# Optimization experiments

Measured on AMD Instinct MI355X. Metric: run time of the kernel, lower is better.

Reference implementation:

```python
import jax, jax.numpy as jnp
import numpy as np
from jax import lax

DIM = 192
NUM_HEADS = 4
HEAD_DIM = DIM // NUM_HEADS
EPS_NORM = 1e-12  # F.normalize default eps
EPS_TEMP = 1e-06


def setup_inputs() -> dict:
    key = jax.random.key(0)
    k1, k2, k3, k4 = jax.random.split(key, 4)
    b, c, h, w = 2, DIM, 192, 192
    x = jax.random.normal(k1, (b, c, h, w), dtype=jnp.float32)
    # conv weights, fan-in scaled for sane magnitudes
    w_qkv = jax.random.normal(k2, (3 * DIM, DIM), dtype=jnp.float32) / np.sqrt(DIM)
    w_dw = jax.random.normal(k3, (3 * DIM, 1, 3, 3), dtype=jnp.float32) / 3.0
    w_proj = jax.random.normal(k4, (DIM, DIM), dtype=jnp.float32) / np.sqrt(DIM)
    log_temperature = jnp.zeros((NUM_HEADS, 1, 1), dtype=jnp.float32)
    return {"x": x, "w_qkv": w_qkv, "w_dw": w_dw, "w_proj": w_proj,
            "log_temperature": log_temperature}


def _l2norm_lastdim(t):
    n = jnp.sqrt(jnp.sum(t * t, axis=-1, keepdims=True))
    return t / jnp.maximum(n, EPS_NORM)


def reference(x, w_qkv, w_dw, w_proj, log_temperature):
    b, c, h, w = x.shape
    hw = h * w
    # 1x1 conv (pointwise GEMM over channels)
    qkv = jnp.einsum('oc,bchw->bohw', w_qkv, x)
    # depthwise 3x3 conv, padding=1
    qkv = lax.conv_general_dilated(
        qkv, w_dw, window_strides=(1, 1), padding='SAME',
        feature_group_count=3 * c,
        dimension_numbers=('NCHW', 'OIHW', 'NCHW'))
    q, k, v = jnp.split(qkv, 3, axis=1)
    # [b, heads, head_dim, hw]
    q = q.reshape(b, NUM_HEADS, HEAD_DIM, hw)
    k = k.reshape(b, NUM_HEADS, HEAD_DIM, hw)
    v = v.reshape(b, NUM_HEADS, HEAD_DIM, hw)
    q = _l2norm_lastdim(q)
    k = _l2norm_lastdim(k)
    # channel-wise attention: [b, heads, head_dim, head_dim]
    attn = jnp.einsum('bhdn,bhen->bhde', q, k)
    temperature = jax.nn.softplus(log_temperature) + EPS_TEMP  # [heads,1,1]
    attn = attn * temperature[None]
    attn = jax.nn.softmax(attn, axis=-1)
    out = jnp.einsum('bhde,bhen->bhdn', attn, v)
    out = out.reshape(b, c, h, w)
    return jnp.einsum('oc,bchw->bohw', w_proj, out)
```

## Files before the change

### kernel.cpp

```cpp
#include <hip/hip_runtime.h>
#include <math.h>

#define HW 36864
#define CC 192

typedef __attribute__((ext_vector_type(4))) float f32x4;
typedef __attribute__((ext_vector_type(8))) short bf16x8;

__device__ __forceinline__ float bf2f(unsigned short u) {
    return __uint_as_float(((unsigned int)u) << 16);
}
__device__ __forceinline__ unsigned short f2bf(float f) {
    unsigned int u = __float_as_uint(f);
    unsigned int r = (u + 0x7fffu + ((u >> 16) & 1u)) >> 16;
    return (unsigned short)r;
}

template<bool OUTBF, int NT, int NZ>
__global__ __launch_bounds__(256, 3) void gemm_rpa(
    const unsigned short* __restrict__ A,
    const unsigned short* __restrict__ X,
    void* __restrict__ Outv,
    long aBatchStride, long xBatchStride, long oBatchStride)
{
    const int nx = gridDim.x;
    int bx = blockIdx.x;
    if ((nx & 7) == 0) {
        const int cpx = nx >> 3;
        bx = (bx & 7) * cpx + (bx >> 3);
    }
    const int z  = (NZ > 1) ? (bx % NZ) : 0;
    const int ng = (NZ > 1) ? (bx / NZ) : bx;
    const int b  = blockIdx.y;
    const int mbase = z * 192;
    const int n00 = ng * (NT * 64);

    const int tid = threadIdx.x;
    const int lane = tid & 63;
    const int wave = tid >> 6;
    const int ml = lane & 15, qk = lane >> 4;
    const int kp = tid & 31;
    const int nc = tid >> 5;

    __shared__ __attribute__((aligned(16))) unsigned short Xs[64 * 202];

    const unsigned short* Ab = A + (long)b * aBatchStride;
    bf16x8 afr[3][6];
#pragma unroll
    for (int f = 0; f < 3; ++f) {
        const unsigned short* row = Ab + (long)(mbase + wave * 48 + f * 16 + ml) * 192 + qk * 8;
#pragma unroll
        for (int kk = 0; kk < 6; ++kk)
            afr[f][kk] = *(const bf16x8*)(row + kk * 32);
    }

    const unsigned short* Xg = X + (long)b * xBatchStride + n00 + nc * 8;

    f32x4 acc[3][4];
#pragma unroll
    for (int f = 0; f < 3; ++f)
#pragma unroll
        for (int s = 0; s < 4; ++s)
            acc[f][s] = (f32x4){0.f, 0.f, 0.f, 0.f};

    auto LOAD = [&](int g, int4* r) {
        const int t = g / 3, sec = g - 3 * t;
        const unsigned short* p = Xg + (long)(sec * 64 + 2 * kp) * HW + t * 64;
        r[0] = *(const int4*)(p);
        r[1] = *(const int4*)(p + HW);
    };
    auto WRITE = [&](int g, const int4* r) {
        const int t = g / 3, sec = g - 3 * t;
        const int k = sec * 64 + 2 * kp;
        const unsigned short* u0 = (const unsigned short*)&r[0];
        const unsigned short* u1 = (const unsigned short*)&r[1];
#pragma unroll
        for (int j = 0; j < 8; ++j)
            *(unsigned int*)&Xs[(nc * 8 + j) * 202 + k] =
                (unsigned int)u0[j] | ((unsigned int)u1[j] << 16);
    };
    auto COMPUTE = [&](int g) {
        const int sec = g % 3;
#pragma unroll
        for (int s = 0; s < 4; ++s) {
#pragma unroll
            for (int kl = 0; kl < 2; ++kl) {
                bf16x8 bfr;
                {
                    const unsigned short* p = &Xs[(s * 16 + ml) * 202 + sec * 64 + kl * 32 + qk * 8];
                    union { bf16x8 v; unsigned int u[4]; } tmp;
                    tmp.u[0] = *(const unsigned int*)(p + 0);
                    tmp.u[1] = *(const unsigned int*)(p + 2);
                    tmp.u[2] = *(const unsigned int*)(p + 4);
                    tmp.u[3] = *(const unsigned int*)(p + 6);
                    bfr = tmp.v;
                }
#pragma unroll
                for (int f = 0; f < 3; ++f)
                    acc[f][s] = __builtin_amdgcn_mfma_f32_16x16x32_bf16(afr[f][sec * 2 + kl], bfr, acc[f][s], 0, 0, 0);
            }
        }
    };
    auto STORE = [&](int t) {
        const int n0 = n00 + t * 64;
#pragma unroll
        for (int f = 0; f < 3; ++f) {
#pragma unroll
            for (int s = 0; s < 4; ++s) {
                const int gm = mbase + wave * 48 + f * 16 + qk * 4;
                const int gn = n0 + s * 16 + ml;
#pragma unroll
                for (int i = 0; i < 4; ++i) {
                    if (OUTBF)
                        ((unsigned short*)Outv)[(long)b * oBatchStride + (long)(gm + i) * HW + gn] = f2bf(acc[f][s][i]);
                    else
                        ((float*)Outv)[(long)b * oBatchStride + (long)(gm + i) * HW + gn] = acc[f][s][i];
                }
                acc[f][s] = (f32x4){0.f, 0.f, 0.f, 0.f};
            }
        }
    };

    constexpr int NS = NT * 3;
    int4 sA[2], sB[2];

    LOAD(0, sA);
    WRITE(0, sA);
    LOAD(1, sB);
    __syncthreads();

#pragma unroll
    for (int g = 0; g < NS; ++g) {
        if ((g & 1) == 0) {
            if (g + 2 < NS) LOAD(g + 2, sA);
            COMPUTE(g);
            if (g + 1 < NS) WRITE(g + 1, sB);
        } else {
            if (g + 2 < NS) LOAD(g + 2, sB);
            COMPUTE(g);
            if (g + 1 < NS) WRITE(g + 1, sA);
        }
        if (g % 3 == 2) STORE(g / 3);
        if (g + 1 < NS) __syncthreads();
    }
}

__global__ __launch_bounds__(256) void dwconv_kernel(
    const unsigned short* __restrict__ qkv,
    const float* __restrict__ wdw,
    unsigned short* __restrict__ dwout,
    float* __restrict__ ssq)
{
    const int ht = blockIdx.x;
    const int ch = blockIdx.y;
    const int b  = blockIdx.z;
    const int tid = threadIdx.x;
    const int lane = tid & 63;
    const int h0 = ht * 8;
    const int t  = tid & 31;
    const int hh = tid >> 5;
    const bool active = (t < 24);

    const float* wp = wdw + ch * 9;
    const float w00 = wp[0], w01 = wp[1], w02 = wp[2];
    const float w10 = wp[3], w11 = wp[4], w12 = wp[5];
    const float w20 = wp[6], w21 = wp[7], w22 = wp[8];

    const long chbase = (long)(b * 576 + ch) * HW;

    float x[3][8];
#pragma unroll
    for (int dy = 0; dy < 3; ++dy) {
        const int hr = h0 + hh + dy - 1;
        int4 ld = make_int4(0, 0, 0, 0);
        if (active && hr >= 0 && hr < 192)
            ld = *(const int4*)(qkv + chbase + (long)hr * 192 + t * 8);
        const unsigned short* u = (const unsigned short*)&ld;
#pragma unroll
        for (int j = 0; j < 8; ++j) x[dy][j] = bf2f(u[j]);
    }

    float lft[3], rgt[3];
#pragma unroll
    for (int dy = 0; dy < 3; ++dy) {
        float l = __shfl(x[dy][7], lane - 1, 64);
        float r = __shfl(x[dy][0], lane + 1, 64);
        lft[dy] = (t == 0) ? 0.f : l;
        rgt[dy] = (t >= 23) ? 0.f : r;
    }

    float acc[8];
#pragma unroll
    for (int j = 0; j < 8; ++j) {
        float a0 = (j == 0) ? lft[0] : x[0][j - 1];
        float a2 = (j == 7) ? rgt[0] : x[0][j + 1];
        float b0 = (j == 0) ? lft[1] : x[1][j - 1];
        float b2 = (j == 7) ? rgt[1] : x[1][j + 1];
        float c0 = (j == 0) ? lft[2] : x[2][j - 1];
        float c2 = (j == 7) ? rgt[2] : x[2][j + 1];
        acc[j] = w00 * a0 + w01 * x[0][j] + w02 * a2
               + w10 * b0 + w11 * x[1][j] + w12 * b2
               + w20 * c0 + w21 * x[2][j] + w22 * c2;
    }

    if (active) {
        int4 st;
        unsigned short* u = (unsigned short*)&st;
#pragma unroll
        for (int j = 0; j < 8; ++j) u[j] = f2bf(acc[j]);
        *(int4*)(dwout + chbase + (long)(h0 + hh) * 192 + t * 8) = st;
    }

    if (ch < 384) {
        float mysq = 0.f;
        if (active) {
#pragma unroll
            for (int j = 0; j < 8; ++j) mysq += acc[j] * acc[j];
        }
#pragma unroll
        for (int off = 32; off > 0; off >>= 1) mysq += __shfl_xor(mysq, off, 64);
        __shared__ float red[4];
        if (lane == 0) red[tid >> 6] = mysq;
        __syncthreads();
        if (tid == 0) atomicAdd(&ssq[b * 384 + ch], red[0] + red[1] + red[2] + red[3]);
    }
}

__global__ __launch_bounds__(256) void gram_kernel(
    const unsigned short* __restrict__ dwb, float* __restrict__ gram)
{
    const int chunk = blockIdx.x;
    const int bh = blockIdx.y;
    const int b = bh >> 2, h = bh & 3;
    const int tid = threadIdx.x;
    const int wave = tid >> 6;
    const int lane = tid & 63;
    const int row = lane & 15, qk = lane >> 4;
    const long n0 = (long)chunk * 512 + wave * 128;

    const unsigned short* qb = dwb + (long)(b * 576 + h * 48) * HW + n0;
    const unsigned short* kb = dwb + (long)(b * 576 + 192 + h * 48) * HW + n0;

    f32x4 acc[3][3];
#pragma unroll
    for (int f = 0; f < 3; ++f)
#pragma unroll
        for (int g = 0; g < 3; ++g) acc[f][g] = (f32x4){0.f, 0.f, 0.f, 0.f};

#pragma unroll
    for (int kk = 0; kk < 128; kk += 32) {
        const int col = kk + qk * 8;
        bf16x8 aq[3], bk[3];
#pragma unroll
        for (int f = 0; f < 3; ++f) aq[f] = *(const bf16x8*)(qb + (long)(f * 16 + row) * HW + col);
#pragma unroll
        for (int g = 0; g < 3; ++g) bk[g] = *(const bf16x8*)(kb + (long)(g * 16 + row) * HW + col);
#pragma unroll
        for (int f = 0; f < 3; ++f)
#pragma unroll
            for (int g = 0; g < 3; ++g)
                acc[f][g] = __builtin_amdgcn_mfma_f32_16x16x32_bf16(aq[f], bk[g], acc[f][g], 0, 0, 0);
    }

    __shared__ float sg[4][64][37];
#pragma unroll
    for (int f = 0; f < 3; ++f)
#pragma unroll
        for (int g = 0; g < 3; ++g)
#pragma unroll
            for (int i = 0; i < 4; ++i)
                sg[wave][lane][f * 12 + g * 4 + i] = acc[f][g][i];
    __syncthreads();

    const int rl = tid >> 2;
    const int i0 = (tid & 3) * 9;
    const int rrow = rl & 15, rqk = rl >> 4;
    float* gb = gram + bh * 2304;
#pragma unroll
    for (int j = 0; j < 9; ++j) {
        const int idx = i0 + j;
        const float v = sg[0][rl][idx] + sg[1][rl][idx] + sg[2][rl][idx] + sg[3][rl][idx];
        const int f = idx / 12, rem = idx - f * 12, g = rem >> 2, i = rem & 3;
        atomicAdd(&gb[(f * 16 + rqk * 4 + i) * 48 + g * 16 + rrow], v);
    }
}

__global__ __launch_bounds__(64) void attn_kernel(
    const float* __restrict__ gram, const float* __restrict__ ssq,
    const float* __restrict__ lt, float* __restrict__ attn)
{
    const int bh = blockIdx.x;
    const int b = bh >> 2, h = bh & 3;
    const int d = threadIdx.x;
    if (d >= 48) return;
    const float temp = log1pf(expf(lt[h])) + 1e-6f;
    const float invq = 1.f / fmaxf(sqrtf(ssq[b * 384 + h * 48 + d]), 1e-12f);
    float p[48];
    float mx = -1e30f;
#pragma unroll
    for (int e = 0; e < 48; ++e) {
        float invk = 1.f / fmaxf(sqrtf(ssq[b * 384 + 192 + h * 48 + e]), 1e-12f);
        float g = gram[bh * 2304 + d * 48 + e] * invq * invk * temp;
        p[e] = g;
        mx = fmaxf(mx, g);
    }
    float sum = 0.f;
#pragma unroll
    for (int e = 0; e < 48; ++e) { float x = expf(p[e] - mx); p[e] = x; sum += x; }
    const float inv = 1.f / sum;
#pragma unroll
    for (int e = 0; e < 48; ++e) attn[bh * 2304 + d * 48 + e] = p[e] * inv;
}

__global__ __launch_bounds__(192) void mproj_kernel(
    const float* __restrict__ wproj, const float* __restrict__ attn,
    unsigned short* __restrict__ Mb)
{
    const int o = blockIdx.x;
    const int b = blockIdx.y;
    const int he = threadIdx.x;
    const int h = he / 48, e = he - h * 48;
    const float* ar = attn + ((b * 4 + h) * 48) * 48 + e;
    const float* wr = wproj + o * 192 + h * 48;
    float acc = 0.f;
#pragma unroll
    for (int d = 0; d < 48; ++d) acc += wr[d] * ar[d * 48];
    Mb[(long)(b * 192 + o) * 192 + he] = f2bf(acc);
}

__global__ void cvt_bf16_kernel(const float* __restrict__ in,
                                unsigned short* __restrict__ out, int n)
{
    int i = blockIdx.x * 256 + threadIdx.x;
    if (i < n) out[i] = f2bf(in[i]);
}

__global__ __launch_bounds__(256) void cvt_x_kernel(
    const float* __restrict__ in, unsigned short* __restrict__ out)
{
    const long i = ((long)blockIdx.x * 256 + threadIdx.x) * 8;
    float4 a = *(const float4*)(in + i);
    float4 b = *(const float4*)(in + i + 4);
    int4 st;
    unsigned short* u = (unsigned short*)&st;
    u[0] = f2bf(a.x); u[1] = f2bf(a.y); u[2] = f2bf(a.z); u[3] = f2bf(a.w);
    u[4] = f2bf(b.x); u[5] = f2bf(b.y); u[6] = f2bf(b.z); u[7] = f2bf(b.w);
    *(int4*)(out + i) = st;
}

extern "C" void kernel_launch(void* const* d_in, const int* in_sizes, int n_in,
                              void* d_out, int out_size, void* d_ws, size_t ws_size,
                              hipStream_t stream)
{
    const float* x      = (const float*)d_in[0];
    const float* w_qkv  = (const float*)d_in[1];
    const float* w_dw   = (const float*)d_in[2];
    const float* w_proj = (const float*)d_in[3];
    const float* lt     = (const float*)d_in[4];

    char* ws = (char*)d_ws;
    unsigned short* wqkv_b = (unsigned short*)(ws + 0);
    float* gram            = (float*)(ws + 221184);
    float* ssq             = (float*)(ws + 294912);
    float* attn            = (float*)(ws + 297984);
    unsigned short* Mb     = (unsigned short*)(ws + 371712);
    unsigned short* qkvb   = (unsigned short*)(ws + 524288);
    unsigned short* dwb    = (unsigned short*)(ws + 524288 + 84934656ll);
    unsigned short* xbf    = dwb;

    hipMemsetAsync(gram, 0, 73728 + 3072, stream);

    cvt_bf16_kernel<<<dim3((110592 + 255) / 256), 256, 0, stream>>>(w_qkv, wqkv_b, 110592);

    cvt_x_kernel<<<dim3(6912), 256, 0, stream>>>(x, xbf);

    gemm_rpa<true, 3, 3><<<dim3(576, 2), 256, 0, stream>>>(
        wqkv_b, xbf, (void*)qkvb,
        0L, (long)192 * HW, (long)576 * HW);

    dwconv_kernel<<<dim3(24, 576, 2), 256, 0, stream>>>(qkvb, w_dw, dwb, ssq);

    gram_kernel<<<dim3(72, 8), 256, 0, stream>>>(dwb, gram);

    attn_kernel<<<dim3(8), 64, 0, stream>>>(gram, ssq, lt, attn);

    mproj_kernel<<<dim3(192, 2), 192, 0, stream>>>(w_proj, attn, Mb);

    gemm_rpa<false, 2, 1><<<dim3(288, 2), 256, 0, stream>>>(
        Mb, dwb + (long)384 * HW, d_out,
        (long)192 * 192, (long)576 * HW, (long)192 * HW);
}
```

Baseline: 266.6 us.

## Stream rows through a rolling buffer in depthwise conv to cut redundant loads

The depthwise 3x3 kernel now has each 32-lane group process 6 consecutive rows with a rotating 3-row register buffer, instead of one row per thread group that reloads all three input rows. Each thread covers 6 columns using an unaligned 16-byte load (reading 7 values, with one neighbour taken by shuffle), so all 32 lanes are active rather than 24. The grid shrinks sixfold. This is meant to cut the tripled global reads of the qkv intermediate and the idle lanes. The costs are unaligned vector loads, less parallelism across blocks, and 4-byte stores in place of 16-byte ones.

```diff
diff --git a/kernel.cpp b/kernel.cpp
--- a/kernel.cpp
+++ b/kernel.cpp
@@ -6,6 +6,7 @@
 
 typedef __attribute__((ext_vector_type(4))) float f32x4;
 typedef __attribute__((ext_vector_type(8))) short bf16x8;
+typedef int i32x4a4 __attribute__((ext_vector_type(4), aligned(4)));
 
 __device__ __forceinline__ float bf2f(unsigned short u) {
     return __uint_as_float(((unsigned int)u) << 16);
@@ -151,15 +152,14 @@
     unsigned short* __restrict__ dwout,
     float* __restrict__ ssq)
 {
-    const int ht = blockIdx.x;
+    const int rt = blockIdx.x;
     const int ch = blockIdx.y;
     const int b  = blockIdx.z;
     const int tid = threadIdx.x;
     const int lane = tid & 63;
-    const int h0 = ht * 8;
     const int t  = tid & 31;
-    const int hh = tid >> 5;
-    const bool active = (t < 24);
+    const int rowgrp = tid >> 5;
+    const int gh = rt * 48 + rowgrp * 6;
 
     const float* wp = wdw + ch * 9;
     const float w00 = wp[0], w01 = wp[1], w02 = wp[2];
@@ -167,60 +167,64 @@
     const float w20 = wp[6], w21 = wp[7], w22 = wp[8];
 
     const long chbase = (long)(b * 576 + ch) * HW;
-
-    float x[3][8];
-#pragma unroll
-    for (int dy = 0; dy < 3; ++dy) {
-        const int hr = h0 + hh + dy - 1;
-        int4 ld = make_int4(0, 0, 0, 0);
-        if (active && hr >= 0 && hr < 192)
-            ld = *(const int4*)(qkv + chbase + (long)hr * 192 + t * 8);
-        const unsigned short* u = (const unsigned short*)&ld;
-#pragma unroll
-        for (int j = 0; j < 8; ++j) x[dy][j] = bf2f(u[j]);
-    }
-
-    float lft[3], rgt[3];
-#pragma unroll
-    for (int dy = 0; dy < 3; ++dy) {
-        float l = __shfl(x[dy][7], lane - 1, 64);
-        float r = __shfl(x[dy][0], lane + 1, 64);
-        lft[dy] = (t == 0) ? 0.f : l;
-        rgt[dy] = (t >= 23) ? 0.f : r;
-    }
-
-    float acc[8];
-#pragma unroll
-    for (int j = 0; j < 8; ++j) {
-        float a0 = (j == 0) ? lft[0] : x[0][j - 1];
-        float a2 = (j == 7) ? rgt[0] : x[0][j + 1];
-        float b0 = (j == 0) ? lft[1] : x[1][j - 1];
-        float b2 = (j == 7) ? rgt[1] : x[1][j + 1];
-        float c0 = (j == 0) ? lft[2] : x[2][j - 1];
-        float c2 = (j == 7) ? rgt[2] : x[2][j + 1];
-        acc[j] = w00 * a0 + w01 * x[0][j] + w02 * a2
-               + w10 * b0 + w11 * x[1][j] + w12 * b2
-               + w20 * c0 + w21 * x[2][j] + w22 * c2;
-    }
-
-    if (active) {
-        int4 st;
-        unsigned short* u = (unsigned short*)&st;
-#pragma unroll
-        for (int j = 0; j < 8; ++j) u[j] = f2bf(acc[j]);
-        *(int4*)(dwout + chbase + (long)(h0 + hh) * 192 + t * 8) = st;
+    const unsigned short* src = qkv + chbase + t * 6;
+    unsigned short* dst = dwout + chbase + t * 6;
+
+    float rbuf[3][7];
+    float lf[3];
+
+    auto LOADROW = [&](int hr, int sl) {
+        if (hr >= 0 && hr < 192) {
+            i32x4a4 v = *(const i32x4a4*)(src + (long)hr * 192);
+            const unsigned short* u = (const unsigned short*)&v;
+#pragma unroll
+            for (int j = 0; j < 7; ++j) rbuf[sl][j] = bf2f(u[j]);
+            if (t == 31) rbuf[sl][6] = 0.f;
+        } else {
+#pragma unroll
+            for (int j = 0; j < 7; ++j) rbuf[sl][j] = 0.f;
+        }
+        float l = __shfl(rbuf[sl][5], lane - 1, 64);
+        lf[sl] = (t == 0) ? 0.f : l;
+    };
+
+    LOADROW(gh - 1, 0);
+    LOADROW(gh,     1);
+
+    float myssq = 0.f;
+
+#pragma unroll
+    for (int r = 0; r < 6; ++r) {
+        const int sla = r % 3;
+        const int slc = (r + 1) % 3;
+        const int slb = (r + 2) % 3;
+        LOADROW(gh + r + 1, slb);
+
+        float o[6];
+#pragma unroll
+        for (int j = 0; j < 6; ++j) {
+            const float a0 = (j == 0) ? lf[sla] : rbuf[sla][j - 1];
+            const float b0 = (j == 0) ? lf[slc] : rbuf[slc][j - 1];
+            const float c0 = (j == 0) ? lf[slb] : rbuf[slb][j - 1];
+            o[j] = w00 * a0 + w01 * rbuf[sla][j] + w02 * rbuf[sla][j + 1]
+                 + w10 * b0 + w11 * rbuf[slc][j] + w12 * rbuf[slc][j + 1]
+                 + w20 * c0 + w21 * rbuf[slb][j] + w22 * rbuf[slb][j + 1];
+        }
+
+        unsigned int* dp = (unsigned int*)(dst + (long)(gh + r) * 192);
+        dp[0] = (unsigned int)f2bf(o[0]) | ((unsigned int)f2bf(o[1]) << 16);
+        dp[1] = (unsigned int)f2bf(o[2]) | ((unsigned int)f2bf(o[3]) << 16);
+        dp[2] = (unsigned int)f2bf(o[4]) | ((unsigned int)f2bf(o[5]) << 16);
+
+#pragma unroll
+        for (int j = 0; j < 6; ++j) myssq += o[j] * o[j];
     }
 
     if (ch < 384) {
-        float mysq = 0.f;
-        if (active) {
-#pragma unroll
-            for (int j = 0; j < 8; ++j) mysq += acc[j] * acc[j];
-        }
-#pragma unroll
-        for (int off = 32; off > 0; off >>= 1) mysq += __shfl_xor(mysq, off, 64);
+#pragma unroll
+        for (int off = 32; off > 0; off >>= 1) myssq += __shfl_xor(myssq, off, 64);
         __shared__ float red[4];
-        if (lane == 0) red[tid >> 6] = mysq;
+        if (lane == 0) red[tid >> 6] = myssq;
         __syncthreads();
         if (tid == 0) atomicAdd(&ssq[b * 384 + ch], red[0] + red[1] + red[2] + red[3]);
     }
@@ -378,7 +382,7 @@
         wqkv_b, xbf, (void*)qkvb,
         0L, (long)192 * HW, (long)576 * HW);
 
-    dwconv_kernel<<<dim3(24, 576, 2), 256, 0, stream>>>(qkvb, w_dw, dwb, ssq);
+    dwconv_kernel<<<dim3(4, 576, 2), 256, 0, stream>>>(qkvb, w_dw, dwb, ssq);
 
     gram_kernel<<<dim3(72, 8), 256, 0, stream>>>(dwb, gram);
 
```

After: 245.5 us. 7.9% less time.
